# Kernel optimization log

Hardware: AMD Instinct MI355X
Metric: run time of the kernel (lower is better)

Reference implementation:

```python
import jax, jax.numpy as jnp
import numpy as np

B, N, D, R = 512, 1024, 256, 100


def setup_inputs() -> dict:
    key = jax.random.key(0)
    k1, k2, k3, k4 = jax.random.split(key, 4)
    node_feature = jax.random.normal(k1, (B, N, D), dtype=jnp.float32)
    edge_weight = jax.random.randint(k2, (B, N), 0, 2, dtype=jnp.int32)
    relation_label = jax.random.randint(k3, (B,), 0, R, dtype=jnp.int32)
    # nn.Embedding weight, xavier_uniform-style scale
    limit = np.sqrt(6.0 / (R + D)).astype(np.float32)
    relation_matrix = jax.random.uniform(k4, (R, D), dtype=jnp.float32, minval=-limit, maxval=limit)
    return {
        "node_feature": node_feature,
        "edge_weight": edge_weight,
        "relation_label": relation_label,
        "relation_matrix": relation_matrix,
    }


def reference(node_feature, edge_weight, relation_label, relation_matrix):
    # Training path of entity_mention_select, vectorized over the batch.
    # Per entity b: n = node[b][edge[b]==1]  (gather by nonzero mask)
    #   scores = n @ rel[label_b]      -> [M_b]
    #   w = softmax(scores, axis=0)    -> [M_b]
    #   out = w @ n                    -> [D]
    # Masked softmax over the full N axis is mathematically identical to
    # gathering the nonzero entries first (masked slots get weight 0).
    q = relation_matrix[relation_label]                      # [B, D]
    scores = jnp.einsum("bnd,bd->bn", node_feature, q)       # [B, N]
    neg_inf = jnp.finfo(scores.dtype).min
    scores = jnp.where(edge_weight == 1, scores, neg_inf)
    w = jax.nn.softmax(scores, axis=-1)                       # [B, N]
    out = jnp.einsum("bn,bnd->bd", w, node_feature)           # [B, D]
    return out
```

## Files before the change

### kernel.cpp

```cpp
#include <hip/hip_runtime.h>
#include <hip/hip_bf16.h>
#include <math.h>

#define BATCH 512
#define NROWS 1024
#define DDIM  256
#define NWAVES 16
#define RB 8


__device__ __forceinline__ unsigned extract_issue(
    unsigned long long& mask, const float4* __restrict__ nodeb,
    int rowbase, int lane, float4 x[RB])
{
    unsigned valid = 0;
    #pragma unroll
    for (int j = 0; j < RB; ++j) {
        x[j] = make_float4(0.f, 0.f, 0.f, 0.f);
        if (mask) {
            const int r = __ffsll(mask) - 1;
            mask &= (mask - 1);
            valid |= (1u << j);
            x[j] = nodeb[(size_t)(rowbase + r) * (DDIM / 4) + lane];
        }
    }
    return valid;
}

__device__ __forceinline__ void consume(
    unsigned valid, const float4 x[RB], const float4 q,
    float& m, float& l, float4& o)
{
    float s[RB];
    #pragma unroll
    for (int j = 0; j < RB; ++j)
        s[j] = (valid & (1u << j))
             ? fmaf(x[j].x, q.x, fmaf(x[j].y, q.y, fmaf(x[j].z, q.z, x[j].w * q.w)))
             : -INFINITY;

    #pragma unroll
    for (int off = 32; off > 0; off >>= 1) {
        #pragma unroll
        for (int j = 0; j < RB; ++j)
            s[j] += __shfl_xor(s[j], off);
    }

    float mnew = m;
    #pragma unroll
    for (int j = 0; j < RB; ++j) mnew = fmaxf(mnew, s[j]);

    const float scale = __expf(m - mnew);
    float p[RB], psum = 0.f;
    #pragma unroll
    for (int j = 0; j < RB; ++j) { p[j] = __expf(s[j] - mnew); psum += p[j]; }

    l = l * scale + psum;
    o.x *= scale; o.y *= scale; o.z *= scale; o.w *= scale;
    #pragma unroll
    for (int j = 0; j < RB; ++j) {
        o.x = fmaf(p[j], x[j].x, o.x);
        o.y = fmaf(p[j], x[j].y, o.y);
        o.z = fmaf(p[j], x[j].z, o.z);
        o.w = fmaf(p[j], x[j].w, o.w);
    }
    m = mnew;
}

__global__ __launch_bounds__(1024, 4) void attn_pool_kernel(
    const float* __restrict__ node,
    const int*   __restrict__ edge,
    const int*   __restrict__ label,
    const float* __restrict__ rel,
    float*       __restrict__ out)
{
    const int b    = blockIdx.x;
    const int tid  = threadIdx.x;
    const int lane = tid & 63;
    const int wave = tid >> 6;

    const int lab = label[b];
    const float4 q = *(const float4*)(rel + (size_t)lab * DDIM + lane * 4);

    const float4* nodeb = (const float4*)(node + (size_t)b * NROWS * DDIM);

    const int e = edge[(size_t)b * NROWS + tid];
    unsigned long long mask = __ballot(e == 1);
    const int rowbase = wave * 64;

    float  m = -INFINITY;
    float  l = 0.0f;
    float4 o = make_float4(0.f, 0.f, 0.f, 0.f);

    float4 xA[RB], xB[RB];
    unsigned vA = extract_issue(mask, nodeb, rowbase, lane, xA);
    while (vA) {
        const unsigned vB = extract_issue(mask, nodeb, rowbase, lane, xB);
        consume(vA, xA, q, m, l, o);
        if (!vB) break;
        vA = extract_issue(mask, nodeb, rowbase, lane, xA);
        consume(vB, xB, q, m, l, o);
    }

    __shared__ float s_m[NWAVES];
    __shared__ float s_l[NWAVES];
    __shared__ float s_o[NWAVES][DDIM];

    if (lane == 0) { s_m[wave] = m; s_l[wave] = l; }
    *(float4*)&s_o[wave][lane * 4] = o;
    __syncthreads();

    if (tid < DDIM) {
        float M = -INFINITY;
        #pragma unroll
        for (int w = 0; w < NWAVES; ++w) M = fmaxf(M, s_m[w]);
        float L = 0.f, acc = 0.f;
        #pragma unroll
        for (int w = 0; w < NWAVES; ++w) {
            const float sc = __expf(s_m[w] - M);
            L   += s_l[w] * sc;
            acc += s_o[w][tid] * sc;
        }
        out[(size_t)b * DDIM + tid] = acc / L;
    }
}

extern "C" void kernel_launch(void* const* d_in, const int* in_sizes, int n_in,
                              void* d_out, int out_size, void* d_ws, size_t ws_size,
                              hipStream_t stream) {
    const float* node  = (const float*)d_in[0];
    const int*   edge  = (const int*)  d_in[1];
    const int*   label = (const int*)  d_in[2];
    const float* rel   = (const float*)d_in[3];
    float*       out   = (float*)d_out;

    attn_pool_kernel<<<dim3(BATCH), dim3(1024), 0, stream>>>(node, edge, label, rel, out);
}
```

Baseline: 631.3 us.

## Halve waves per block, give each wave 128 rows, make row loads unconditional

Each block now runs 8 waves of 64 lanes, and each wave covers 128 rows using two ballot masks. The extraction loop becomes branch-free: it always issues a load, falling back to a dummy row once both masks are empty, and a validity bitmask excludes those rows. This removes divergent conditional loads and gives each wave longer streams of in-flight loads. The cost is fewer waves per block to hide latency and some redundant loads of dummy rows at the tail.

After: 633.4 us. About the same (+0.3%).

```diff
diff --git a/kernel.cpp b/kernel.cpp
--- a/kernel.cpp
+++ b/kernel.cpp
@@ -1,28 +1,32 @@
 #include <hip/hip_runtime.h>
-#include <hip/hip_bf16.h>
 #include <math.h>
 
 #define BATCH 512
 #define NROWS 1024
 #define DDIM  256
-#define NWAVES 16
-#define RB 8
+#define NWAVES 8
+#define RPW   128
+#define RB    8
 
 
 __device__ __forceinline__ unsigned extract_issue(
-    unsigned long long& mask, const float4* __restrict__ nodeb,
+    unsigned long long& m0, unsigned long long& m1,
+    const float4* __restrict__ nodeb,
     int rowbase, int lane, float4 x[RB])
 {
     unsigned valid = 0;
     #pragma unroll
     for (int j = 0; j < RB; ++j) {
-        x[j] = make_float4(0.f, 0.f, 0.f, 0.f);
-        if (mask) {
-            const int r = __ffsll(mask) - 1;
-            mask &= (mask - 1);
-            valid |= (1u << j);
-            x[j] = nodeb[(size_t)(rowbase + r) * (DDIM / 4) + lane];
-        }
+        const bool h0 = (m0 != 0ULL);
+        const unsigned long long cur = h0 ? m0 : m1;
+        const bool any = (cur != 0ULL);
+        const int  r   = __ffsll(cur) - 1;
+        const int  row = (h0 ? 0 : 64) + (any ? r : 0);
+        const unsigned long long nxt = cur & (cur - 1ULL);
+        m0 = h0 ? nxt : m0;
+        m1 = h0 ? m1  : nxt;
+        valid |= any ? (1u << j) : 0u;
+        x[j] = nodeb[(size_t)(rowbase + row) * (DDIM / 4) + lane];
     }
     return valid;
 }
@@ -66,7 +70,7 @@
     m = mnew;
 }
 
-__global__ __launch_bounds__(1024, 4) void attn_pool_kernel(
+__global__ __launch_bounds__(512, 2) void attn_pool_kernel(
     const float* __restrict__ node,
     const int*   __restrict__ edge,
     const int*   __restrict__ label,
@@ -82,22 +86,23 @@
     const float4 q = *(const float4*)(rel + (size_t)lab * DDIM + lane * 4);
 
     const float4* nodeb = (const float4*)(node + (size_t)b * NROWS * DDIM);
+    const int rowbase = wave * RPW;
 
-    const int e = edge[(size_t)b * NROWS + tid];
-    unsigned long long mask = __ballot(e == 1);
-    const int rowbase = wave * 64;
+    const int* edgeb = edge + (size_t)b * NROWS + rowbase;
+    unsigned long long m0 = __ballot(edgeb[lane]      == 1);
+    unsigned long long m1 = __ballot(edgeb[64 + lane] == 1);
 
     float  m = -INFINITY;
     float  l = 0.0f;
     float4 o = make_float4(0.f, 0.f, 0.f, 0.f);
 
     float4 xA[RB], xB[RB];
-    unsigned vA = extract_issue(mask, nodeb, rowbase, lane, xA);
+    unsigned vA = extract_issue(m0, m1, nodeb, rowbase, lane, xA);
     while (vA) {
-        const unsigned vB = extract_issue(mask, nodeb, rowbase, lane, xB);
+        const unsigned vB = extract_issue(m0, m1, nodeb, rowbase, lane, xB);
         consume(vA, xA, q, m, l, o);
         if (!vB) break;
-        vA = extract_issue(mask, nodeb, rowbase, lane, xA);
+        vA = extract_issue(m0, m1, nodeb, rowbase, lane, xA);
         consume(vB, xB, q, m, l, o);
     }
 
@@ -133,5 +138,5 @@
     const float* rel   = (const float*)d_in[3];
     float*       out   = (float*)d_out;
 
-    attn_pool_kernel<<<dim3(BATCH), dim3(1024), 0, stream>>>(node, edge, label, rel, out);
+    attn_pool_kernel<<<dim3(BATCH), dim3(512), 0, stream>>>(node, edge, label, rel, out);
 }
```
